# Optimization experiments

Measured on AMD Instinct MI355X. Metric: run time of the kernel, lower is better.

Reference implementation:

```python
import jax, jax.numpy as jnp
import numpy as np

C = 512
GROUPS = 16
EPS = 1e-6


def group_norm(x, gamma, beta):
    # x: (b, c, h, w)
    b, c, h, w = x.shape
    xg = x.reshape(b, GROUPS, c // GROUPS, h, w)
    mean = xg.mean(axis=(2, 3, 4), keepdims=True)
    var = xg.var(axis=(2, 3, 4), keepdims=True)
    xn = ((xg - mean) * jax.lax.rsqrt(var + EPS)).reshape(b, c, h, w)
    return xn * gamma[None, :, None, None] + beta[None, :, None, None]


def setup_inputs() -> dict:
    key = jax.random.key(0)
    ks = jax.random.split(key, 9)
    scale = 1.0 / np.sqrt(C)
    x = jax.random.normal(ks[0], (32, C, 32, 32), dtype=jnp.float32)
    return {
        "x": x,
        "gn_gamma": jnp.ones((C,), jnp.float32),
        "gn_beta": jnp.zeros((C,), jnp.float32),
        "wq": jax.random.normal(ks[1], (C, C), jnp.float32) * scale,
        "bq": jnp.zeros((C,), jnp.float32),
        "wk": jax.random.normal(ks[2], (C, C), jnp.float32) * scale,
        "bk": jnp.zeros((C,), jnp.float32),
        "wv": jax.random.normal(ks[3], (C, C), jnp.float32) * scale,
        "bv": jnp.zeros((C,), jnp.float32),
        "wp": jax.random.normal(ks[4], (C, C), jnp.float32) * scale,
        "bp": jnp.zeros((C,), jnp.float32),
    }


def reference(x, gn_gamma, gn_beta, wq, bq, wk, bk, wv, bv, wp, bp):
    b, c, h, w = x.shape
    hn = group_norm(x, gn_gamma, gn_beta).reshape(b, c, h * w)  # (b, c, n)
    # 1x1 convs == per-token channel GEMMs
    q = jnp.einsum('oc,bcn->bon', wq, hn) + bq[None, :, None]
    k = jnp.einsum('oc,bcn->bon', wk, hn) + bk[None, :, None]
    v = jnp.einsum('oc,bcn->bon', wv, hn) + bv[None, :, None]
    # scores: (b, n, m) = q^T k, scaled
    s = jnp.einsum('bcn,bcm->bnm', q, k) * (float(c) ** -0.5)
    # original subtracts the global max (shift-invariant) then softmax over dim 2
    s = s - jnp.max(s)
    attn = jax.nn.softmax(s, axis=2)
    # h_ = v @ attn^T  -> (b, c, n)
    out = jnp.einsum('bcm,bnm->bcn', v, attn)
    out = jnp.einsum('oc,bcn->bon', wp, out) + bp[None, :, None]
    return x + out.reshape(b, c, h, w)
```

## Files before the change

kernel.cpp:

```cpp
#include <hip/hip_runtime.h>
#include <hip/hip_bf16.h>

typedef unsigned short u16;
typedef __attribute__((ext_vector_type(8))) short bf16x8;
typedef __attribute__((ext_vector_type(4))) float f32x4;

#define BK 32
#define TILE_U16 (128 * BK)

__device__ __forceinline__ u16 f2bf(float f) {
  union { float f; unsigned u; } a; a.f = f;
  unsigned r = a.u + 0x7fffu + ((a.u >> 16) & 1u);
  return (u16)(r >> 16);
}

__device__ __forceinline__ u16 f2h(float f) {
  union { _Float16 h; u16 u; } c; c.h = (_Float16)f; return c.u;
}

__device__ __forceinline__ void stage_async(const u16* __restrict__ g, int ldg,
                                            u16* __restrict__ s, int tid) {
  int lane = tid & 63, wave = tid >> 6;
  int chunk = wave * 64 + lane;
  int row = chunk >> 2;
  int kc = (chunk - (row >> 1)) & 3;
  __builtin_amdgcn_global_load_lds(
      (const __attribute__((address_space(1))) unsigned int*)(g + (long)row * ldg + kc * 8),
      (__attribute__((address_space(3))) unsigned int*)(s + wave * 512),
      16, 0, 0);
}

__device__ __forceinline__ void gemm_core(
    const u16* __restrict__ Ab, const u16* __restrict__ Bb,
    int lda, int ldb, int K, int tid,
    u16* __restrict__ As, u16* __restrict__ Bs, f32x4 (&acc)[2][4]) {
  int lane = tid & 63, wave = tid >> 6;
  int wr = wave >> 1, wc = wave & 1;
  int lrow = lane & 15, quad = lane >> 4;
  int aoff[2], boff[4];
#pragma unroll
  for (int mt = 0; mt < 2; ++mt) {
    int row = wr * 32 + mt * 16 + lrow;
    aoff[mt] = row * BK + ((quad + (row >> 1)) & 3) * 8;
  }
#pragma unroll
  for (int nt = 0; nt < 4; ++nt) {
    int row = wc * 64 + nt * 16 + lrow;
    boff[nt] = row * BK + ((quad + (row >> 1)) & 3) * 8;
  }
#pragma unroll
  for (int i = 0; i < 2; ++i)
#pragma unroll
    for (int j = 0; j < 4; ++j) acc[i][j] = (f32x4){0.f, 0.f, 0.f, 0.f};

  stage_async(Ab, lda, As, tid);
  stage_async(Bb, ldb, Bs, tid);
  int cur = 0;
  for (int k0 = 0; k0 < K; k0 += BK) {
    __syncthreads();
    if (k0 + BK < K) {
      stage_async(Ab + k0 + BK, lda, As + (cur ^ 1) * TILE_U16, tid);
      stage_async(Bb + k0 + BK, ldb, Bs + (cur ^ 1) * TILE_U16, tid);
    }
    const u16* Ac = As + cur * TILE_U16;
    const u16* Bc = Bs + cur * TILE_U16;
    bf16x8 af[2], bfr[4];
#pragma unroll
    for (int mt = 0; mt < 2; ++mt) af[mt] = *(const bf16x8*)&Ac[aoff[mt]];
#pragma unroll
    for (int nt = 0; nt < 4; ++nt) bfr[nt] = *(const bf16x8*)&Bc[boff[nt]];
#pragma unroll
    for (int mt = 0; mt < 2; ++mt)
#pragma unroll
      for (int nt = 0; nt < 4; ++nt)
        acc[mt][nt] = __builtin_amdgcn_mfma_f32_16x16x32_bf16(af[mt], bfr[nt], acc[mt][nt], 0, 0, 0);
    cur ^= 1;
  }
}

template <bool FP16>
__device__ __forceinline__ void epi_trans(
    f32x4 (&acc)[2][4], u16* __restrict__ C, long cbase, int m0, int n0, int ldc,
    const float* __restrict__ bias, float scale, int tid) {
  int lane = tid & 63, wave = tid >> 6;
  int wr = wave >> 1, wc = wave & 1;
  int lrow = lane & 15, quad = lane >> 4;
#pragma unroll
  for (int mt = 0; mt < 2; ++mt) {
    int rowbase = m0 + wr * 32 + mt * 16 + quad * 4;
    float4 b4 = bias ? *(const float4*)&bias[rowbase] : make_float4(0.f, 0.f, 0.f, 0.f);
#pragma unroll
    for (int nt = 0; nt < 4; ++nt) {
      int col = n0 + wc * 64 + nt * 16 + lrow;
      f32x4 a = acc[mt][nt];
      float v0 = a[0] * scale + b4.x, v1 = a[1] * scale + b4.y;
      float v2 = a[2] * scale + b4.z, v3 = a[3] * scale + b4.w;
      uint2 o;
      if (FP16) {
        o.x = (unsigned)f2h(v0) | ((unsigned)f2h(v1) << 16);
        o.y = (unsigned)f2h(v2) | ((unsigned)f2h(v3) << 16);
      } else {
        o.x = (unsigned)f2bf(v0) | ((unsigned)f2bf(v1) << 16);
        o.y = (unsigned)f2bf(v2) | ((unsigned)f2bf(v3) << 16);
      }
      *(uint2*)(C + cbase + (long)col * ldc + rowbase) = o;
    }
  }
}

template <int MODE>
__global__ __launch_bounds__(512, 4) void gemm_kernel(
    const u16* __restrict__ Ag, const u16* __restrict__ Bg,
    void* __restrict__ C0, void* __restrict__ C1, void* __restrict__ C2,
    const float* __restrict__ bias0, const float* __restrict__ bias1,
    const float* __restrict__ bias2, const float* __restrict__ resid,
    int lda, int ldb, int ldc,
    long strideA, long strideB, long strideC, int K, float scale) {
  __shared__ u16 As[2 * TILE_U16];
  __shared__ u16 Bs[2 * TILE_U16];
  int tid = threadIdx.x;
  int b = blockIdx.z;
  int m0 = blockIdx.y * 128, n0 = blockIdx.x * 128;
  const u16* Ab = Ag + (long)b * strideA + (long)m0 * lda;
  const u16* Bb = Bg + (long)b * strideB + (long)n0 * ldb;
  f32x4 acc[2][4];
  gemm_core(Ab, Bb, lda, ldb, K, tid, As, Bs, acc);

  int lane = tid & 63, wave = tid >> 6;
  int wr = wave >> 1, wc = wave & 1;
  int lrow = lane & 15, quad = lane >> 4;
  long cbase = (long)b * strideC;

  if (MODE == 0) {
    epi_trans<false>(acc, (u16*)C0, cbase, m0, n0, ldc, bias0, scale, tid);
  } else if (MODE == 1) {
    epi_trans<true>(acc, (u16*)C0, cbase, m0, n0, ldc, nullptr, scale, tid);
  } else if (MODE == 2) {
#pragma unroll
    for (int mt = 0; mt < 2; ++mt)
#pragma unroll
      for (int r = 0; r < 4; ++r) {
        int row = m0 + wr * 32 + mt * 16 + quad * 4 + r;
        float bv = bias0[row];
#pragma unroll
        for (int nt = 0; nt < 4; ++nt) {
          int col = n0 + wc * 64 + nt * 16 + lrow;
          long idx = cbase + (long)row * ldc + col;
          ((float*)C0)[idx] = acc[mt][nt][r] * scale + bv + resid[idx];
        }
      }
  } else {
    int seg = m0 >> 9;
    int ml = m0 & 511;
    if (seg == 0) {
      epi_trans<false>(acc, (u16*)C0, cbase, ml, n0, 512, bias0, 1.f, tid);
    } else if (seg == 1) {
      epi_trans<false>(acc, (u16*)C1, cbase, ml, n0, 512, bias1, 1.f, tid);
    } else {
#pragma unroll
      for (int mt = 0; mt < 2; ++mt)
#pragma unroll
        for (int r = 0; r < 4; ++r) {
          int row = ml + wr * 32 + mt * 16 + quad * 4 + r;
          float bv = bias2[row];
#pragma unroll
          for (int nt = 0; nt < 4; ++nt) {
            int col = n0 + wc * 64 + nt * 16 + lrow;
            ((u16*)C2)[cbase + (long)row * 1024 + col] = f2bf(acc[mt][nt][r] + bv);
          }
        }
    }
  }
}

__global__ __launch_bounds__(256) void groupnorm_kernel(
    const float* __restrict__ x, const float* __restrict__ gamma,
    const float* __restrict__ beta, u16* __restrict__ hnT) {
  int g = blockIdx.x, b = blockIdx.y;
  const float* xb = x + ((long)b * 512 + g * 32) * 1024;
  int tid = threadIdx.x;
  float s = 0.f, sq = 0.f;
  float4 vals[32];
#pragma unroll
  for (int j = 0; j < 32; ++j) {
    float4 v = *(const float4*)(xb + (long)j * 1024 + tid * 4);
    vals[j] = v;
    s += v.x + v.y + v.z + v.w;
    sq += v.x * v.x + v.y * v.y + v.z * v.z + v.w * v.w;
  }
#pragma unroll
  for (int off = 1; off < 64; off <<= 1) {
    s += __shfl_xor(s, off);
    sq += __shfl_xor(sq, off);
  }
  __shared__ float ls[4], lq[4];
  if ((tid & 63) == 0) { ls[tid >> 6] = s; lq[tid >> 6] = sq; }
  __syncthreads();
  float ts = ls[0] + ls[1] + ls[2] + ls[3];
  float tq = lq[0] + lq[1] + lq[2] + lq[3];
  float mean = ts * (1.f / 32768.f);
  float var = tq * (1.f / 32768.f) - mean * mean;
  float rstd = rsqrtf(var + 1e-6f);
  u16* hb = hnT + (long)b * (1024 * 512) + g * 32;
#pragma unroll
  for (int t = 0; t < 4; ++t) {
    u16 row[32];
#pragma unroll
    for (int j = 0; j < 32; ++j) {
      float xv = ((const float*)&vals[j])[t];
      row[j] = f2bf((xv - mean) * rstd * gamma[g * 32 + j] + beta[g * 32 + j]);
    }
    uint4* dst = (uint4*)(hb + (long)(tid * 4 + t) * 512);
    const uint4* src = (const uint4*)row;
    dst[0] = src[0]; dst[1] = src[1]; dst[2] = src[2]; dst[3] = src[3];
  }
}

__global__ __launch_bounds__(256) void softmax_kernel(u16* __restrict__ s) {
  long row = blockIdx.x;
  u16* sr = s + row * 1024;
  int tid = threadIdx.x;
  union { uint2 u; _Float16 h[4]; } c;
  c.u = *(const uint2*)(sr + tid * 4);
  float v0 = (float)c.h[0], v1 = (float)c.h[1], v2 = (float)c.h[2], v3 = (float)c.h[3];
  float m = fmaxf(fmaxf(v0, v1), fmaxf(v2, v3));
#pragma unroll
  for (int off = 1; off < 64; off <<= 1) m = fmaxf(m, __shfl_xor(m, off));
  __shared__ float lm[4], lsum[4];
  if ((tid & 63) == 0) lm[tid >> 6] = m;
  __syncthreads();
  float rowmax = fmaxf(fmaxf(lm[0], lm[1]), fmaxf(lm[2], lm[3]));
  float e0 = expf(v0 - rowmax), e1 = expf(v1 - rowmax);
  float e2 = expf(v2 - rowmax), e3 = expf(v3 - rowmax);
  float sum = e0 + e1 + e2 + e3;
#pragma unroll
  for (int off = 1; off < 64; off <<= 1) sum += __shfl_xor(sum, off);
  if ((tid & 63) == 0) lsum[tid >> 6] = sum;
  __syncthreads();
  float inv = 1.f / (lsum[0] + lsum[1] + lsum[2] + lsum[3]);
  uint2 o;
  o.x = (unsigned)f2bf(e0 * inv) | ((unsigned)f2bf(e1 * inv) << 16);
  o.y = (unsigned)f2bf(e2 * inv) | ((unsigned)f2bf(e3 * inv) << 16);
  *(uint2*)(sr + tid * 4) = o;
}

__global__ __launch_bounds__(256) void convertw_kernel(
    const float* __restrict__ w0, const float* __restrict__ w1,
    const float* __restrict__ w2, const float* __restrict__ w3,
    u16* __restrict__ out) {
  int wsel = blockIdx.x >> 8;
  const float* src = wsel == 0 ? w0 : wsel == 1 ? w1 : wsel == 2 ? w2 : w3;
  int idx = ((blockIdx.x & 255) * 256 + threadIdx.x) * 4;
  float4 v = *(const float4*)(src + idx);
  uint2 o;
  o.x = (unsigned)f2bf(v.x) | ((unsigned)f2bf(v.y) << 16);
  o.y = (unsigned)f2bf(v.z) | ((unsigned)f2bf(v.w) << 16);
  *(uint2*)(out + (long)wsel * 262144 + idx) = o;
}

extern "C" void kernel_launch(void* const* d_in, const int* in_sizes, int n_in,
                              void* d_out, int out_size, void* d_ws, size_t ws_size,
                              hipStream_t stream) {
  const float* x     = (const float*)d_in[0];
  const float* gamma = (const float*)d_in[1];
  const float* beta  = (const float*)d_in[2];
  const float* wq    = (const float*)d_in[3];
  const float* bq    = (const float*)d_in[4];
  const float* wk    = (const float*)d_in[5];
  const float* bk    = (const float*)d_in[6];
  const float* wv    = (const float*)d_in[7];
  const float* bv    = (const float*)d_in[8];
  const float* wp    = (const float*)d_in[9];
  const float* bp    = (const float*)d_in[10];
  float* out = (float*)d_out;
  char* ws = (char*)d_ws;

  u16* wbf = (u16*)ws;
  u16* hnT = (u16*)(ws + (2L << 20));
  u16* qT  = (u16*)(ws + (34L << 20));
  u16* kT  = (u16*)(ws + (66L << 20));
  u16* v   = (u16*)(ws + (98L << 20));
  u16* s16 = (u16*)(ws + (130L << 20));
  u16* aoT = hnT;

  const long SB = 512L * 1024;
  const long SS = 1024L * 1024;
  const float scale = 0.044194173824159216f;

  convertw_kernel<<<1024, 256, 0, stream>>>(wq, wk, wv, wp, wbf);
  groupnorm_kernel<<<dim3(16, 32), 256, 0, stream>>>(x, gamma, beta, hnT);

  gemm_kernel<3><<<dim3(8, 12, 32), 512, 0, stream>>>(
      wbf, hnT, qT, kT, v, bq, bk, bv, nullptr,
      512, 512, 0, 0, SB, SB, 512, 1.f);

  gemm_kernel<1><<<dim3(8, 8, 32), 512, 0, stream>>>(
      kT, qT, s16, nullptr, nullptr, nullptr, nullptr, nullptr, nullptr,
      512, 512, 1024, SB, SB, SS, 512, scale);

  softmax_kernel<<<32 * 1024, 256, 0, stream>>>(s16);

  gemm_kernel<0><<<dim3(8, 4, 32), 512, 0, stream>>>(
      v, s16, aoT, nullptr, nullptr, nullptr, nullptr, nullptr, nullptr,
      1024, 1024, 512, SB, SS, SB, 1024, 1.f);

  gemm_kernel<2><<<dim3(8, 4, 32), 512, 0, stream>>>(
      wbf + 3 * 262144, aoT, out, nullptr, nullptr, bp, nullptr, nullptr, x,
      512, 512, 1024, 0, SB, SB, 512, 1.f);
}
```

Before: 425.3 us.

## Fuse QK^T, softmax and PV into a single flash-attention kernel

Replaces the separate score GEMM, row-softmax kernel and attention-value GEMM with one online-softmax flash kernel. Per query tile it streams K and V through LDS, keeps running max and sum, and accumulates the full 512-channel output in registers. This removes the write and read of the fp16 score matrix and two kernel launches. In exchange the grid is only 256 blocks, each with a large register footprint, many block-wide barriers per tile, and reduced parallelism compared with the separate GEMMs.

```diff
diff --git a/kernel.cpp b/kernel.cpp
--- a/kernel.cpp
+++ b/kernel.cpp
@@ -12,10 +12,6 @@
   union { float f; unsigned u; } a; a.f = f;
   unsigned r = a.u + 0x7fffu + ((a.u >> 16) & 1u);
   return (u16)(r >> 16);
-}
-
-__device__ __forceinline__ u16 f2h(float f) {
-  union { _Float16 h; u16 u; } c; c.h = (_Float16)f; return c.u;
 }
 
 __device__ __forceinline__ void stage_async(const u16* __restrict__ g, int ldg,
@@ -30,6 +26,221 @@
       16, 0, 0);
 }
 
+template <int NCH>
+__device__ __forceinline__ void stage_rows(const u16* __restrict__ g, int ldg,
+                                           u16* __restrict__ s, int tid) {
+#pragma unroll
+  for (int c0 = 0; c0 < NCH; c0 += 512) {
+    int c = c0 + tid;
+    int row = c >> 2;
+    int kc = (c - (row >> 1)) & 3;
+    __builtin_amdgcn_global_load_lds(
+        (const __attribute__((address_space(1))) unsigned int*)(g + (long)row * ldg + kc * 8),
+        (__attribute__((address_space(3))) unsigned int*)(s + (c0 + (tid & ~63)) * 8),
+        16, 0, 0);
+  }
+}
+
+__global__ __launch_bounds__(512, 2) void flash_kernel(
+    const u16* __restrict__ qT, const u16* __restrict__ kT,
+    const u16* __restrict__ vN, u16* __restrict__ aoT) {
+  __shared__ __align__(16) u16 stg[2][8192];
+  __shared__ __align__(16) u16 Plds[16384];
+  float* fov = (float*)&stg[1][0];
+
+  const int tid = threadIdx.x;
+  const int lane = tid & 63, wave = tid >> 6;
+  const int lrow = lane & 15, quad = lane >> 4;
+  const int wg = wave >> 1, wh = wave & 1;
+  const int b = blockIdx.y, qt = blockIdx.x;
+  const long SB = 512L * 1024;
+  const u16* qb = qT + (long)b * SB + (long)(qt * 128) * 512;
+  const u16* kb = kT + (long)b * SB;
+  const u16* vb = vN + (long)b * SB;
+  const float scale = 0.044194173824159216f;
+
+  int aq[2], bkf[4], av[4], qc[4];
+#pragma unroll
+  for (int mt = 0; mt < 2; ++mt) { int r = wg * 32 + mt * 16 + lrow; aq[mt] = r * 32 + ((quad + (r >> 1)) & 3) * 8; }
+#pragma unroll
+  for (int nt = 0; nt < 4; ++nt) { int r = wh * 64 + nt * 16 + lrow; bkf[nt] = 4096 + r * 32 + ((quad + (r >> 1)) & 3) * 8; }
+#pragma unroll
+  for (int mt = 0; mt < 4; ++mt) { int r = wg * 64 + mt * 16 + lrow; av[mt] = r * 32 + ((quad + (r >> 1)) & 3) * 8; }
+#pragma unroll
+  for (int nt = 0; nt < 4; ++nt) qc[nt] = wh * 64 + nt * 16 + lrow;
+
+  float m_r = -INFINITY, l_r = 0.f;
+  f32x4 acc_o[2][4][4];
+#pragma unroll
+  for (int h = 0; h < 2; ++h)
+#pragma unroll
+    for (int mt = 0; mt < 4; ++mt)
+#pragma unroll
+      for (int nt = 0; nt < 4; ++nt) acc_o[h][mt][nt] = (f32x4){0.f, 0.f, 0.f, 0.f};
+
+  stage_rows<512>(qb, 512, stg[0], tid);
+  stage_rows<512>(kb, 512, stg[0] + 4096, tid);
+
+  for (int t = 0; t < 8; ++t) {
+    const u16* kbt = kb + (long)t * (128 * 512);
+    f32x4 acc_s[2][4];
+#pragma unroll
+    for (int mt = 0; mt < 2; ++mt)
+#pragma unroll
+      for (int nt = 0; nt < 4; ++nt) acc_s[mt][nt] = (f32x4){0.f, 0.f, 0.f, 0.f};
+
+    for (int c = 0; c < 16; ++c) {
+      __syncthreads();
+      int buf = c & 1;
+      if (c < 15) {
+        stage_rows<512>(qb + (c + 1) * 32, 512, stg[buf ^ 1], tid);
+        stage_rows<512>(kbt + (c + 1) * 32, 512, stg[buf ^ 1] + 4096, tid);
+      }
+      bf16x8 af[2], bf[4];
+#pragma unroll
+      for (int mt = 0; mt < 2; ++mt) af[mt] = *(const bf16x8*)&stg[buf][aq[mt]];
+#pragma unroll
+      for (int nt = 0; nt < 4; ++nt) bf[nt] = *(const bf16x8*)&stg[buf][bkf[nt]];
+#pragma unroll
+      for (int mt = 0; mt < 2; ++mt)
+#pragma unroll
+        for (int nt = 0; nt < 4; ++nt)
+          acc_s[mt][nt] = __builtin_amdgcn_mfma_f32_16x16x32_bf16(af[mt], bf[nt], acc_s[mt][nt], 0, 0, 0);
+    }
+    __syncthreads();
+
+#pragma unroll
+    for (int mt = 0; mt < 2; ++mt)
+#pragma unroll
+      for (int nt = 0; nt < 4; ++nt) acc_s[mt][nt] *= scale;
+    float rmax[2][4];
+#pragma unroll
+    for (int mt = 0; mt < 2; ++mt)
+#pragma unroll
+      for (int r = 0; r < 4; ++r) {
+        float m0 = fmaxf(acc_s[mt][0][r], acc_s[mt][1][r]);
+        float m1 = fmaxf(acc_s[mt][2][r], acc_s[mt][3][r]);
+        rmax[mt][r] = fmaxf(m0, m1);
+      }
+#pragma unroll
+    for (int off = 1; off < 16; off <<= 1)
+#pragma unroll
+      for (int mt = 0; mt < 2; ++mt)
+#pragma unroll
+        for (int r = 0; r < 4; ++r) rmax[mt][r] = fmaxf(rmax[mt][r], __shfl_xor(rmax[mt][r], off));
+    if (lrow == 0) {
+#pragma unroll
+      for (int mt = 0; mt < 2; ++mt)
+#pragma unroll
+        for (int r = 0; r < 4; ++r)
+          fov[(wg * 32 + mt * 16 + quad * 4 + r) * 2 + wh] = rmax[mt][r];
+    }
+    stage_rows<1024>(vb + t * 128, 1024, stg[0], tid);
+    __syncthreads();
+
+    float alpha_r = 0.f;
+    if (tid < 128) {
+      float mt_ = fmaxf(fov[tid * 2], fov[tid * 2 + 1]);
+      float mnew = fmaxf(m_r, mt_);
+      alpha_r = __expf(m_r - mnew);
+      m_r = mnew;
+      fov[512 + tid] = mnew;
+      fov[640 + tid] = alpha_r;
+    }
+    __syncthreads();
+
+    float psum[2][4];
+#pragma unroll
+    for (int mt = 0; mt < 2; ++mt)
+#pragma unroll
+      for (int r = 0; r < 4; ++r) psum[mt][r] = 0.f;
+#pragma unroll
+    for (int mt = 0; mt < 2; ++mt)
+#pragma unroll
+      for (int r = 0; r < 4; ++r) {
+        int row = wg * 32 + mt * 16 + quad * 4 + r;
+        float mn = fov[512 + row];
+#pragma unroll
+        for (int nt = 0; nt < 4; ++nt) {
+          float p = __expf(acc_s[mt][nt][r] - mn);
+          psum[mt][r] += p;
+          int key = wh * 64 + nt * 16 + lrow;
+          Plds[row * 128 + (((key >> 3) + row) & 15) * 8 + (key & 7)] = f2bf(p);
+        }
+      }
+#pragma unroll
+    for (int off = 1; off < 16; off <<= 1)
+#pragma unroll
+      for (int mt = 0; mt < 2; ++mt)
+#pragma unroll
+        for (int r = 0; r < 4; ++r) psum[mt][r] += __shfl_xor(psum[mt][r], off);
+    if (lrow == 0) {
+#pragma unroll
+      for (int mt = 0; mt < 2; ++mt)
+#pragma unroll
+        for (int r = 0; r < 4; ++r)
+          fov[256 + (wg * 32 + mt * 16 + quad * 4 + r) * 2 + wh] = psum[mt][r];
+    }
+    __syncthreads();
+
+    if (tid < 128) l_r = alpha_r * l_r + fov[256 + tid * 2] + fov[256 + tid * 2 + 1];
+    float a4[4];
+#pragma unroll
+    for (int nt = 0; nt < 4; ++nt) a4[nt] = fov[640 + qc[nt]];
+#pragma unroll
+    for (int h = 0; h < 2; ++h)
+#pragma unroll
+      for (int mt = 0; mt < 4; ++mt)
+#pragma unroll
+        for (int nt = 0; nt < 4; ++nt) acc_o[h][mt][nt] *= a4[nt];
+
+    for (int j = 0; j < 8; ++j) {
+      __syncthreads();
+      if (j < 7) {
+        int jn = j + 1;
+        stage_rows<1024>(vb + (long)((jn >> 2) * 256) * 1024 + t * 128 + (jn & 3) * 32,
+                         1024, stg[jn & 1], tid);
+      } else if (t < 7) {
+        stage_rows<512>(qb, 512, stg[0], tid);
+        stage_rows<512>(kbt + 128 * 512, 512, stg[0] + 4096, tid);
+      }
+      int half = j >> 2, cc = j & 3;
+      bf16x8 afv[4], bfp[4];
+#pragma unroll
+      for (int mt = 0; mt < 4; ++mt) afv[mt] = *(const bf16x8*)&stg[j & 1][av[mt]];
+#pragma unroll
+      for (int nt = 0; nt < 4; ++nt)
+        bfp[nt] = *(const bf16x8*)&Plds[qc[nt] * 128 + (((cc * 4 + quad) + qc[nt]) & 15) * 8];
+#pragma unroll
+      for (int mt = 0; mt < 4; ++mt)
+#pragma unroll
+        for (int nt = 0; nt < 4; ++nt)
+          acc_o[half][mt][nt] = __builtin_amdgcn_mfma_f32_16x16x32_bf16(afv[mt], bfp[nt], acc_o[half][mt][nt], 0, 0, 0);
+    }
+  }
+
+  __syncthreads();
+  if (tid < 128) fov[tid] = 1.f / l_r;
+  __syncthreads();
+  float li[4];
+#pragma unroll
+  for (int nt = 0; nt < 4; ++nt) li[nt] = fov[qc[nt]];
+#pragma unroll
+  for (int h = 0; h < 2; ++h)
+#pragma unroll
+    for (int mt = 0; mt < 4; ++mt)
+#pragma unroll
+      for (int nt = 0; nt < 4; ++nt) {
+        f32x4 o = acc_o[h][mt][nt];
+        int ch = h * 256 + wg * 64 + mt * 16 + quad * 4;
+        long idx = (long)b * SB + (long)(qt * 128 + qc[nt]) * 512 + ch;
+        uint2 st;
+        st.x = (unsigned)f2bf(o[0] * li[nt]) | ((unsigned)f2bf(o[1] * li[nt]) << 16);
+        st.y = (unsigned)f2bf(o[2] * li[nt]) | ((unsigned)f2bf(o[3] * li[nt]) << 16);
+        *(uint2*)&aoT[idx] = st;
+      }
+}
+
 __device__ __forceinline__ void gemm_core(
     const u16* __restrict__ Ab, const u16* __restrict__ Bb,
     int lda, int ldb, int K, int tid,
@@ -78,10 +289,9 @@
   }
 }
 
-template <bool FP16>
-__device__ __forceinline__ void epi_trans(
+__device__ __forceinline__ void epi_trans_bf16(
     f32x4 (&acc)[2][4], u16* __restrict__ C, long cbase, int m0, int n0, int ldc,
-    const float* __restrict__ bias, float scale, int tid) {
+    const float* __restrict__ bias, int tid) {
   int lane = tid & 63, wave = tid >> 6;
   int wr = wave >> 1, wc = wave & 1;
   int lrow = lane & 15, quad = lane >> 4;
@@ -93,16 +303,9 @@
     for (int nt = 0; nt < 4; ++nt) {
       int col = n0 + wc * 64 + nt * 16 + lrow;
       f32x4 a = acc[mt][nt];
-      float v0 = a[0] * scale + b4.x, v1 = a[1] * scale + b4.y;
-      float v2 = a[2] * scale + b4.z, v3 = a[3] * scale + b4.w;
       uint2 o;
-      if (FP16) {
-        o.x = (unsigned)f2h(v0) | ((unsigned)f2h(v1) << 16);
-        o.y = (unsigned)f2h(v2) | ((unsigned)f2h(v3) << 16);
-      } else {
-        o.x = (unsigned)f2bf(v0) | ((unsigned)f2bf(v1) << 16);
-        o.y = (unsigned)f2bf(v2) | ((unsigned)f2bf(v3) << 16);
-      }
+      o.x = (unsigned)f2bf(a[0] + b4.x) | ((unsigned)f2bf(a[1] + b4.y) << 16);
+      o.y = (unsigned)f2bf(a[2] + b4.z) | ((unsigned)f2bf(a[3] + b4.w) << 16);
       *(uint2*)(C + cbase + (long)col * ldc + rowbase) = o;
     }
   }
@@ -115,9 +318,9 @@
     const float* __restrict__ bias0, const float* __restrict__ bias1,
     const float* __restrict__ bias2, const float* __restrict__ resid,
     int lda, int ldb, int ldc,
-    long strideA, long strideB, long strideC, int K, float scale) {
-  __shared__ u16 As[2 * TILE_U16];
-  __shared__ u16 Bs[2 * TILE_U16];
+    long strideA, long strideB, long strideC, int K) {
+  __shared__ __align__(16) u16 As[2 * TILE_U16];
+  __shared__ __align__(16) u16 Bs[2 * TILE_U16];
   int tid = threadIdx.x;
   int b = blockIdx.z;
   int m0 = blockIdx.y * 128, n0 = blockIdx.x * 128;
@@ -131,11 +334,7 @@
   int lrow = lane & 15, quad = lane >> 4;
   long cbase = (long)b * strideC;
 
-  if (MODE == 0) {
-    epi_trans<false>(acc, (u16*)C0, cbase, m0, n0, ldc, bias0, scale, tid);
-  } else if (MODE == 1) {
-    epi_trans<true>(acc, (u16*)C0, cbase, m0, n0, ldc, nullptr, scale, tid);
-  } else if (MODE == 2) {
+  if (MODE == 2) {
 #pragma unroll
     for (int mt = 0; mt < 2; ++mt)
 #pragma unroll
@@ -146,16 +345,16 @@
         for (int nt = 0; nt < 4; ++nt) {
           int col = n0 + wc * 64 + nt * 16 + lrow;
           long idx = cbase + (long)row * ldc + col;
-          ((float*)C0)[idx] = acc[mt][nt][r] * scale + bv + resid[idx];
+          ((float*)C0)[idx] = acc[mt][nt][r] + bv + resid[idx];
         }
       }
   } else {
     int seg = m0 >> 9;
     int ml = m0 & 511;
     if (seg == 0) {
-      epi_trans<false>(acc, (u16*)C0, cbase, ml, n0, 512, bias0, 1.f, tid);
+      epi_trans_bf16(acc, (u16*)C0, cbase, ml, n0, 512, bias0, tid);
     } else if (seg == 1) {
-      epi_trans<false>(acc, (u16*)C1, cbase, ml, n0, 512, bias1, 1.f, tid);
+      epi_trans_bf16(acc, (u16*)C1, cbase, ml, n0, 512, bias1, tid);
     } else {
 #pragma unroll
       for (int mt = 0; mt < 2; ++mt)
@@ -214,34 +413,6 @@
     const uint4* src = (const uint4*)row;
     dst[0] = src[0]; dst[1] = src[1]; dst[2] = src[2]; dst[3] = src[3];
   }
-}
-
-__global__ __launch_bounds__(256) void softmax_kernel(u16* __restrict__ s) {
-  long row = blockIdx.x;
-  u16* sr = s + row * 1024;
-  int tid = threadIdx.x;
-  union { uint2 u; _Float16 h[4]; } c;
-  c.u = *(const uint2*)(sr + tid * 4);
-  float v0 = (float)c.h[0], v1 = (float)c.h[1], v2 = (float)c.h[2], v3 = (float)c.h[3];
-  float m = fmaxf(fmaxf(v0, v1), fmaxf(v2, v3));
-#pragma unroll
-  for (int off = 1; off < 64; off <<= 1) m = fmaxf(m, __shfl_xor(m, off));
-  __shared__ float lm[4], lsum[4];
-  if ((tid & 63) == 0) lm[tid >> 6] = m;
-  __syncthreads();
-  float rowmax = fmaxf(fmaxf(lm[0], lm[1]), fmaxf(lm[2], lm[3]));
-  float e0 = expf(v0 - rowmax), e1 = expf(v1 - rowmax);
-  float e2 = expf(v2 - rowmax), e3 = expf(v3 - rowmax);
-  float sum = e0 + e1 + e2 + e3;
-#pragma unroll
-  for (int off = 1; off < 64; off <<= 1) sum += __shfl_xor(sum, off);
-  if ((tid & 63) == 0) lsum[tid >> 6] = sum;
-  __syncthreads();
-  float inv = 1.f / (lsum[0] + lsum[1] + lsum[2] + lsum[3]);
-  uint2 o;
-  o.x = (unsigned)f2bf(e0 * inv) | ((unsigned)f2bf(e1 * inv) << 16);
-  o.y = (unsigned)f2bf(e2 * inv) | ((unsigned)f2bf(e3 * inv) << 16);
-  *(uint2*)(sr + tid * 4) = o;
 }
 
 __global__ __launch_bounds__(256) void convertw_kernel(
@@ -280,31 +451,20 @@
   u16* qT  = (u16*)(ws + (34L << 20));
   u16* kT  = (u16*)(ws + (66L << 20));
   u16* v   = (u16*)(ws + (98L << 20));
-  u16* s16 = (u16*)(ws + (130L << 20));
   u16* aoT = hnT;
 
   const long SB = 512L * 1024;
-  const long SS = 1024L * 1024;
-  const float scale = 0.044194173824159216f;
 
   convertw_kernel<<<1024, 256, 0, stream>>>(wq, wk, wv, wp, wbf);
   groupnorm_kernel<<<dim3(16, 32), 256, 0, stream>>>(x, gamma, beta, hnT);
 
   gemm_kernel<3><<<dim3(8, 12, 32), 512, 0, stream>>>(
       wbf, hnT, qT, kT, v, bq, bk, bv, nullptr,
-      512, 512, 0, 0, SB, SB, 512, 1.f);
-
-  gemm_kernel<1><<<dim3(8, 8, 32), 512, 0, stream>>>(
-      kT, qT, s16, nullptr, nullptr, nullptr, nullptr, nullptr, nullptr,
-      512, 512, 1024, SB, SB, SS, 512, scale);
-
-  softmax_kernel<<<32 * 1024, 256, 0, stream>>>(s16);
-
-  gemm_kernel<0><<<dim3(8, 4, 32), 512, 0, stream>>>(
-      v, s16, aoT, nullptr, nullptr, nullptr, nullptr, nullptr, nullptr,
-      1024, 1024, 512, SB, SS, SB, 1024, 1.f);
+      512, 512, 0, 0, SB, SB, 512);
+
+  flash_kernel<<<dim3(8, 32), 512, 0, stream>>>(qT, kT, v, aoT);
 
   gemm_kernel<2><<<dim3(8, 4, 32), 512, 0, stream>>>(
       wbf + 3 * 262144, aoT, out, nullptr, nullptr, bp, nullptr, nullptr, x,
-      512, 512, 1024, 0, SB, SB, 512, 1.f);
-}
+      512, 512, 1024, 0, SB, SB, 512);
+}
```

New measurement: 510.7 us. 20.1% more time.
